# Kernel optimization log

Hardware: AMD Instinct MI355X
Metric: run time of the kernel (lower is better)

Reference implementation:

```python
import jax, jax.numpy as jnp
import numpy as np

N_NODES = 4096
N_EDGES = 500000
N_PAIRS = 2000000
EDGE_DIM = 16
MAX_PATH = 5


def setup_inputs() -> dict:
    key = jax.random.key(0)
    k1, k2, k3, k4, k5 = jax.random.split(key, 5)
    x = jax.random.normal(k1, (N_NODES, EDGE_DIM), dtype=jnp.float32)
    edge_attr = jax.random.normal(k2, (N_EDGES, EDGE_DIM), dtype=jnp.float32)
    path_idx = jax.random.randint(k3, (N_PAIRS, MAX_PATH), 0, N_EDGES, dtype=jnp.int64)
    path_lens = jax.random.randint(k4, (N_PAIRS,), 0, MAX_PATH + 1, dtype=jnp.int64)
    pair_id = jnp.arange(N_PAIRS, dtype=jnp.int64)
    # learned parameter: edge_weights [max_path_distance, edge_dim]
    edge_weights = jax.random.normal(k5, (MAX_PATH, EDGE_DIM), dtype=jnp.float32)
    return {"x": x, "edge_attr": edge_attr, "edge_weights": edge_weights,
            "path_idx": path_idx, "path_lens": path_lens, "pair_id": pair_id}


def reference(x, edge_attr, edge_weights, path_idx, path_lens, pair_id):
    N = x.shape[0]
    L = edge_weights.shape[0]  # max_path_distance
    # valid-position mask for each ragged path, padded to length L
    mask = (jnp.arange(L)[None, :] < path_lens[:, None]).astype(edge_attr.dtype)  # [P, L]
    gathered = edge_attr[path_idx]  # [P, L, D] ragged gather of edge features
    # per-hop dot with learned per-hop weight vector, i.e. (w_l * e_l).sum(dim=1)
    dots = jnp.einsum('pld,ld->pl', gathered, edge_weights)  # [P, L]
    s = jnp.sum(dots * mask, axis=1)  # [P]
    cnt = path_lens.astype(edge_attr.dtype)
    # mean over valid hops; empty path -> NaN in torch -> nan_to_num -> 0
    mean = jnp.where(cnt > 0, s / jnp.maximum(cnt, 1.0), jnp.zeros_like(s))
    src = pair_id % N
    dst = pair_id // N  # unique (src, dst) pairs by construction
    cij = jnp.zeros((N, N), dtype=edge_attr.dtype).at[src, dst].set(mean)
    return cij
```

## Files before the change

kernel.cpp:

```cpp
#include <hip/hip_runtime.h>
#include <hip/hip_fp16.h>

#define NNODES 4096
#define NEDGES 500000
#define NPAIRS 2000000
#define EDIM   16
#define LMAX   5

typedef int v4i __attribute__((ext_vector_type(4)));
typedef float v4f __attribute__((ext_vector_type(4)));

__device__ __forceinline__ v4i ntload4(const int* p) {
  return __builtin_nontemporal_load((const v4i*)p);
}
__device__ __forceinline__ void ntstore4(float* p, float x, float y, float z, float w) {
  v4f t = {x, y, z, w};
  __builtin_nontemporal_store(t, (v4f*)p);
}

#define GLL(gp, lp) __builtin_amdgcn_global_load_lds(                      \
    (const __attribute__((address_space(1))) uint32_t*)(gp),               \
    (__attribute__((address_space(3))) uint32_t*)(lp), 4, 0, 0)

#define DBLOCKS ((NEDGES / 2 + 255) / 256)
#define ZBLOCKS 16384

__global__ __launch_bounds__(256) void prep_kernel(
    const float* __restrict__ edge_attr,
    const float* __restrict__ ew,
    __half* __restrict__ dots,
    float* __restrict__ out) {
  __shared__ float w[LMAX * EDIM];
  const int tid = threadIdx.x, bid = blockIdx.x;

  if (bid >= DBLOCKS) {
    int z = bid - DBLOCKS;
    ntstore4(out + ((size_t)z * 256 + tid) * 4, 0.f, 0.f, 0.f, 0.f);
    return;
  }

  if (tid < LMAX * EDIM) w[tid] = ew[tid];
  __syncthreads();

  int e0 = (bid * 256 + tid) * 2;
  if (e0 >= NEDGES) return;

  const float4* ra = (const float4*)(edge_attr + (size_t)e0 * EDIM);
  float4 a0 = ra[0], a1 = ra[1], a2 = ra[2], a3 = ra[3];
  float4 b0 = ra[4], b1 = ra[5], b2 = ra[6], b3 = ra[7];
  float va[16] = {a0.x, a0.y, a0.z, a0.w, a1.x, a1.y, a1.z, a1.w,
                  a2.x, a2.y, a2.z, a2.w, a3.x, a3.y, a3.z, a3.w};
  float vb[16] = {b0.x, b0.y, b0.z, b0.w, b1.x, b1.y, b1.z, b1.w,
                  b2.x, b2.y, b2.z, b2.w, b3.x, b3.y, b3.z, b3.w};
#pragma unroll
  for (int l = 0; l < LMAX; ++l) {
    float da = 0.f, db = 0.f;
#pragma unroll
    for (int k = 0; k < EDIM; ++k) {
      da += va[k] * w[l * EDIM + k];
      db += vb[k] * w[l * EDIM + k];
    }
    __half2 h;
    h.x = __float2half(da);
    h.y = __float2half(db);
    *(__half2*)(dots + (size_t)l * NEDGES + e0) = h;
  }
}

__device__ __forceinline__ void issue5(const uint32_t* gdots, uint32_t* lbase,
                                       int len, int i0, int i1, int i2, int i3, int i4) {
  uint32_t e0 = (len > 0) ? (uint32_t)i0 : 0u;
  uint32_t e1 = (len > 1) ? (uint32_t)(1 * NEDGES + i1) : 0u;
  uint32_t e2 = (len > 2) ? (uint32_t)(2 * NEDGES + i2) : 0u;
  uint32_t e3 = (len > 3) ? (uint32_t)(3 * NEDGES + i3) : 0u;
  uint32_t e4 = (len > 4) ? (uint32_t)(4 * NEDGES + i4) : 0u;
  GLL(gdots + (e0 >> 1), lbase + 0 * 64);
  GLL(gdots + (e1 >> 1), lbase + 1 * 64);
  GLL(gdots + (e2 >> 1), lbase + 2 * 64);
  GLL(gdots + (e3 >> 1), lbase + 3 * 64);
  GLL(gdots + (e4 >> 1), lbase + 4 * 64);
}

__device__ __forceinline__ float pick(uint32_t dw, int elem) {
  unsigned short u = (unsigned short)((elem & 1) ? (dw >> 16) : (dw & 0xffffu));
  return __half2float(__ushort_as_half(u));
}

__device__ __forceinline__ float sum5(const uint32_t* lbase, int lane, int len,
                                      int i0, int i1, int i2, int i3, int i4) {
  float v0 = pick(lbase[0 * 64 + lane], i0);
  float v1 = pick(lbase[1 * 64 + lane], i1);
  float v2 = pick(lbase[2 * 64 + lane], i2);
  float v3 = pick(lbase[3 * 64 + lane], i3);
  float v4 = pick(lbase[4 * 64 + lane], i4);
  float s = (((len > 0) ? v0 : 0.f) + ((len > 1) ? v1 : 0.f)) +
            (((len > 2) ? v2 : 0.f) + ((len > 3) ? v3 : 0.f)) +
            ((len > 4) ? v4 : 0.f);
  return s / (float)max(len, 1);
}

#define NHEAVY 1024

__global__ __launch_bounds__(256, 3) void fused_mean_transpose(
    const int* __restrict__ path_idx,
    const int* __restrict__ path_lens,
    const __half* __restrict__ dots,
    float* __restrict__ out) {
  __shared__ float tile[64][33];
  __shared__ uint32_t gbuf[4][40][64];
  const int bid = blockIdx.x;
  const int tid = threadIdx.x;
  const int wave = tid >> 6, lane = tid & 63;

  const int tt = bid >> 1;
  const int h  = bid & 1;
  const int dst0 = (tt & 7) * 64 + h * 32;
  const int src0 = (tt >> 3) * 64;
  const uint32_t* gdots = (const uint32_t*)dots;

  {
    const int a = tid >> 4;
    const int c = tid & 15;
    int p0 = (dst0 + a) * NNODES + src0 + 4 * c;
    int p1 = p0 + 16 * NNODES;
    float valid0 = (p0 < NPAIRS) ? 1.f : 0.f;
    float valid1 = (p1 < NPAIRS) ? 1.f : 0.f;
    int pc0 = min(p0, NPAIRS - 4);
    int pc1 = min(p1, NPAIRS - 4);

    const int* q0 = path_idx + (size_t)pc0 * LMAX;
    const int* q1 = path_idx + (size_t)pc1 * LMAX;
    v4i ln0 = ntload4(path_lens + pc0);
    v4i A0 = ntload4(q0);
    v4i B0 = ntload4(q0 + 4);
    v4i C0 = ntload4(q0 + 8);
    v4i D0 = ntload4(q0 + 12);
    v4i E0 = ntload4(q0 + 16);
    v4i ln1 = ntload4(path_lens + pc1);
    v4i A1 = ntload4(q1);
    v4i B1 = ntload4(q1 + 4);
    v4i C1 = ntload4(q1 + 8);
    v4i D1 = ntload4(q1 + 12);
    v4i E1 = ntload4(q1 + 16);
    __builtin_amdgcn_sched_barrier(0);

    int L0 = min(max(ln0[0], 0), LMAX), L1 = min(max(ln0[1], 0), LMAX);
    int L2 = min(max(ln0[2], 0), LMAX), L3 = min(max(ln0[3], 0), LMAX);
    int L4 = min(max(ln1[0], 0), LMAX), L5 = min(max(ln1[1], 0), LMAX);
    int L6 = min(max(ln1[2], 0), LMAX), L7 = min(max(ln1[3], 0), LMAX);

    issue5(gdots, &gbuf[wave][0][0],  L0, A0[0], A0[1], A0[2], A0[3], B0[0]);
    issue5(gdots, &gbuf[wave][5][0],  L1, B0[1], B0[2], B0[3], C0[0], C0[1]);
    issue5(gdots, &gbuf[wave][10][0], L2, C0[2], C0[3], D0[0], D0[1], D0[2]);
    issue5(gdots, &gbuf[wave][15][0], L3, D0[3], E0[0], E0[1], E0[2], E0[3]);
    issue5(gdots, &gbuf[wave][20][0], L4, A1[0], A1[1], A1[2], A1[3], B1[0]);
    issue5(gdots, &gbuf[wave][25][0], L5, B1[1], B1[2], B1[3], C1[0], C1[1]);
    issue5(gdots, &gbuf[wave][30][0], L6, C1[2], C1[3], D1[0], D1[1], D1[2]);
    issue5(gdots, &gbuf[wave][35][0], L7, D1[3], E1[0], E1[1], E1[2], E1[3]);
    asm volatile("s_waitcnt vmcnt(0)" ::: "memory");
    __builtin_amdgcn_sched_barrier(0);

    float4 v0, v1;
    v0.x = sum5(&gbuf[wave][0][0],  lane, L0, A0[0], A0[1], A0[2], A0[3], B0[0]) * valid0;
    v0.y = sum5(&gbuf[wave][5][0],  lane, L1, B0[1], B0[2], B0[3], C0[0], C0[1]) * valid0;
    v0.z = sum5(&gbuf[wave][10][0], lane, L2, C0[2], C0[3], D0[0], D0[1], D0[2]) * valid0;
    v0.w = sum5(&gbuf[wave][15][0], lane, L3, D0[3], E0[0], E0[1], E0[2], E0[3]) * valid0;
    v1.x = sum5(&gbuf[wave][20][0], lane, L4, A1[0], A1[1], A1[2], A1[3], B1[0]) * valid1;
    v1.y = sum5(&gbuf[wave][25][0], lane, L5, B1[1], B1[2], B1[3], C1[0], C1[1]) * valid1;
    v1.z = sum5(&gbuf[wave][30][0], lane, L6, C1[2], C1[3], D1[0], D1[1], D1[2]) * valid1;
    v1.w = sum5(&gbuf[wave][35][0], lane, L7, D1[3], E1[0], E1[1], E1[2], E1[3]) * valid1;

    tile[4 * c + 0][a] = v0.x;
    tile[4 * c + 1][a] = v0.y;
    tile[4 * c + 2][a] = v0.z;
    tile[4 * c + 3][a] = v0.w;
    tile[4 * c + 0][a + 16] = v1.x;
    tile[4 * c + 1][a + 16] = v1.y;
    tile[4 * c + 2][a + 16] = v1.z;
    tile[4 * c + 3][a + 16] = v1.w;
  }
  __syncthreads();
  {
    const int r  = tid >> 2;
    const int cc = tid & 3;
    float x0 = tile[r][4 * cc + 0];
    float y0 = tile[r][4 * cc + 1];
    float z0 = tile[r][4 * cc + 2];
    float w0 = tile[r][4 * cc + 3];
    float x1 = tile[r][16 + 4 * cc + 0];
    float y1 = tile[r][16 + 4 * cc + 1];
    float z1 = tile[r][16 + 4 * cc + 2];
    float w1 = tile[r][16 + 4 * cc + 3];
    float* o = out + (size_t)(src0 + r) * NNODES + dst0;
    ntstore4(o + 4 * cc, x0, y0, z0, w0);
    ntstore4(o + 16 + 4 * cc, x1, y1, z1, w1);
  }
}

__global__ __launch_bounds__(256) void scatter_kernel(
    const float* __restrict__ edge_attr,
    const float* __restrict__ ew,
    const int* __restrict__ path_idx,
    const int* __restrict__ path_lens,
    float* __restrict__ out) {
  __shared__ float w[LMAX * EDIM];
  if (threadIdx.x < LMAX * EDIM) w[threadIdx.x] = ew[threadIdx.x];
  __syncthreads();

  int p = blockIdx.x * 256 + threadIdx.x;
  if (p >= NPAIRS) return;

  int len = path_lens[p];
  len = min(max(len, 0), LMAX);

  const int* row = path_idx + (size_t)p * LMAX;
  float s = 0.f;
  for (int l = 0; l < len; ++l) {
    int idx = row[l];
    const float4* r = (const float4*)(edge_attr + (size_t)idx * EDIM);
    float4 a0 = r[0], a1 = r[1], a2 = r[2], a3 = r[3];
    const float* wl = &w[l * EDIM];
    s += a0.x * wl[0] + a0.y * wl[1] + a0.z * wl[2] + a0.w * wl[3] +
         a1.x * wl[4] + a1.y * wl[5] + a1.z * wl[6] + a1.w * wl[7] +
         a2.x * wl[8] + a2.y * wl[9] + a2.z * wl[10] + a2.w * wl[11] +
         a3.x * wl[12] + a3.y * wl[13] + a3.z * wl[14] + a3.w * wl[15];
  }
  float m = (len > 0) ? (s / (float)len) : 0.f;
  int src = p & (NNODES - 1);
  int dst = p >> 12;
  out[(size_t)src * NNODES + dst] = m;
}

extern "C" void kernel_launch(void* const* d_in, const int* in_sizes, int n_in,
                              void* d_out, int out_size, void* d_ws, size_t ws_size,
                              hipStream_t stream) {
  const float* edge_attr = (const float*)d_in[1];
  const float* edge_w    = (const float*)d_in[2];
  const int*   path_idx  = (const int*)d_in[3];
  const int*   path_lens = (const int*)d_in[4];
  float* out = (float*)d_out;

  const size_t need = (size_t)LMAX * NEDGES * sizeof(__half);

  if (ws_size >= need) {
    __half* dots = (__half*)d_ws;

    prep_kernel<<<DBLOCKS + ZBLOCKS, 256, 0, stream>>>(edge_attr, edge_w, dots, out);
    fused_mean_transpose<<<NHEAVY, 256, 0, stream>>>(path_idx, path_lens, dots, out);
  } else {
    hipMemsetAsync(d_out, 0, (size_t)out_size * sizeof(float), stream);
    scatter_kernel<<<(NPAIRS + 255) / 256, 256, 0, stream>>>(
        edge_attr, edge_w, path_idx, path_lens, out);
  }
}
```

Baseline: 174.8 us.

## Double-buffer per-hop dot gathers into LDS to shrink shared memory footprint

Replaces the one-shot issue of all 40 global-to-LDS gathers per wave with a hop-by-hop loop. Each loop step issues 8 gathers into one of two LDS buffers while the previous hop is consumed, using a partial vmcnt wait. This cuts the per-wave LDS buffer from 40 to 16 rows, and the launch bound is raised to 4 blocks per CU for more occupancy. The cost is serialized latency across the 5 hops and extra waits, which could lower memory-level parallelism per wave.

```diff
diff --git a/kernel.cpp b/kernel.cpp
--- a/kernel.cpp
+++ b/kernel.cpp
@@ -67,47 +67,15 @@
   }
 }
 
-__device__ __forceinline__ void issue5(const uint32_t* gdots, uint32_t* lbase,
-                                       int len, int i0, int i1, int i2, int i3, int i4) {
-  uint32_t e0 = (len > 0) ? (uint32_t)i0 : 0u;
-  uint32_t e1 = (len > 1) ? (uint32_t)(1 * NEDGES + i1) : 0u;
-  uint32_t e2 = (len > 2) ? (uint32_t)(2 * NEDGES + i2) : 0u;
-  uint32_t e3 = (len > 3) ? (uint32_t)(3 * NEDGES + i3) : 0u;
-  uint32_t e4 = (len > 4) ? (uint32_t)(4 * NEDGES + i4) : 0u;
-  GLL(gdots + (e0 >> 1), lbase + 0 * 64);
-  GLL(gdots + (e1 >> 1), lbase + 1 * 64);
-  GLL(gdots + (e2 >> 1), lbase + 2 * 64);
-  GLL(gdots + (e3 >> 1), lbase + 3 * 64);
-  GLL(gdots + (e4 >> 1), lbase + 4 * 64);
-}
-
-__device__ __forceinline__ float pick(uint32_t dw, int elem) {
-  unsigned short u = (unsigned short)((elem & 1) ? (dw >> 16) : (dw & 0xffffu));
-  return __half2float(__ushort_as_half(u));
-}
-
-__device__ __forceinline__ float sum5(const uint32_t* lbase, int lane, int len,
-                                      int i0, int i1, int i2, int i3, int i4) {
-  float v0 = pick(lbase[0 * 64 + lane], i0);
-  float v1 = pick(lbase[1 * 64 + lane], i1);
-  float v2 = pick(lbase[2 * 64 + lane], i2);
-  float v3 = pick(lbase[3 * 64 + lane], i3);
-  float v4 = pick(lbase[4 * 64 + lane], i4);
-  float s = (((len > 0) ? v0 : 0.f) + ((len > 1) ? v1 : 0.f)) +
-            (((len > 2) ? v2 : 0.f) + ((len > 3) ? v3 : 0.f)) +
-            ((len > 4) ? v4 : 0.f);
-  return s / (float)max(len, 1);
-}
-
 #define NHEAVY 1024
 
-__global__ __launch_bounds__(256, 3) void fused_mean_transpose(
+__global__ __launch_bounds__(256, 4) void fused_mean_transpose(
     const int* __restrict__ path_idx,
     const int* __restrict__ path_lens,
     const __half* __restrict__ dots,
     float* __restrict__ out) {
   __shared__ float tile[64][33];
-  __shared__ uint32_t gbuf[4][40][64];
+  __shared__ uint32_t gbuf[4][2][8][64];
   const int bid = blockIdx.x;
   const int tid = threadIdx.x;
   const int wave = tid >> 6, lane = tid & 63;
@@ -142,33 +110,69 @@
     v4i C1 = ntload4(q1 + 8);
     v4i D1 = ntload4(q1 + 12);
     v4i E1 = ntload4(q1 + 16);
-    __builtin_amdgcn_sched_barrier(0);
-
-    int L0 = min(max(ln0[0], 0), LMAX), L1 = min(max(ln0[1], 0), LMAX);
-    int L2 = min(max(ln0[2], 0), LMAX), L3 = min(max(ln0[3], 0), LMAX);
-    int L4 = min(max(ln1[0], 0), LMAX), L5 = min(max(ln1[1], 0), LMAX);
-    int L6 = min(max(ln1[2], 0), LMAX), L7 = min(max(ln1[3], 0), LMAX);
-
-    issue5(gdots, &gbuf[wave][0][0],  L0, A0[0], A0[1], A0[2], A0[3], B0[0]);
-    issue5(gdots, &gbuf[wave][5][0],  L1, B0[1], B0[2], B0[3], C0[0], C0[1]);
-    issue5(gdots, &gbuf[wave][10][0], L2, C0[2], C0[3], D0[0], D0[1], D0[2]);
-    issue5(gdots, &gbuf[wave][15][0], L3, D0[3], E0[0], E0[1], E0[2], E0[3]);
-    issue5(gdots, &gbuf[wave][20][0], L4, A1[0], A1[1], A1[2], A1[3], B1[0]);
-    issue5(gdots, &gbuf[wave][25][0], L5, B1[1], B1[2], B1[3], C1[0], C1[1]);
-    issue5(gdots, &gbuf[wave][30][0], L6, C1[2], C1[3], D1[0], D1[1], D1[2]);
-    issue5(gdots, &gbuf[wave][35][0], L7, D1[3], E1[0], E1[1], E1[2], E1[3]);
+
+    int f[8][LMAX];
+#pragma unroll
+    for (int k = 0; k < 4; ++k) {
+      f[0][k] = A0[k]; f[4][k] = A1[k];
+      f[1][k + 1] = B0[k + 1 > 3 ? 0 : 0], f[1][k] = 0;
+    }
+    f[0][0]=A0[0]; f[0][1]=A0[1]; f[0][2]=A0[2]; f[0][3]=A0[3]; f[0][4]=B0[0];
+    f[1][0]=B0[1]; f[1][1]=B0[2]; f[1][2]=B0[3]; f[1][3]=C0[0]; f[1][4]=C0[1];
+    f[2][0]=C0[2]; f[2][1]=C0[3]; f[2][2]=D0[0]; f[2][3]=D0[1]; f[2][4]=D0[2];
+    f[3][0]=D0[3]; f[3][1]=E0[0]; f[3][2]=E0[1]; f[3][3]=E0[2]; f[3][4]=E0[3];
+    f[4][0]=A1[0]; f[4][1]=A1[1]; f[4][2]=A1[2]; f[4][3]=A1[3]; f[4][4]=B1[0];
+    f[5][0]=B1[1]; f[5][1]=B1[2]; f[5][2]=B1[3]; f[5][3]=C1[0]; f[5][4]=C1[1];
+    f[6][0]=C1[2]; f[6][1]=C1[3]; f[6][2]=D1[0]; f[6][3]=D1[1]; f[6][4]=D1[2];
+    f[7][0]=D1[3]; f[7][1]=E1[0]; f[7][2]=E1[1]; f[7][3]=E1[2]; f[7][4]=E1[3];
+
+    int L[8];
+    L[0]=min(max(ln0[0],0),LMAX); L[1]=min(max(ln0[1],0),LMAX);
+    L[2]=min(max(ln0[2],0),LMAX); L[3]=min(max(ln0[3],0),LMAX);
+    L[4]=min(max(ln1[0],0),LMAX); L[5]=min(max(ln1[1],0),LMAX);
+    L[6]=min(max(ln1[2],0),LMAX); L[7]=min(max(ln1[3],0),LMAX);
+
     asm volatile("s_waitcnt vmcnt(0)" ::: "memory");
-    __builtin_amdgcn_sched_barrier(0);
+
+#pragma unroll
+    for (int j = 0; j < 8; ++j) {
+      uint32_t e = (L[j] > 0) ? (uint32_t)f[j][0] : 0u;
+      GLL(gdots + (e >> 1), &gbuf[wave][0][j][0]);
+    }
+    float s[8] = {0.f, 0.f, 0.f, 0.f, 0.f, 0.f, 0.f, 0.f};
+#pragma unroll
+    for (int l = 0; l < LMAX; ++l) {
+      if (l + 1 < LMAX) {
+#pragma unroll
+        for (int j = 0; j < 8; ++j) {
+          uint32_t e = (L[j] > l + 1)
+              ? (uint32_t)((l + 1) * NEDGES + f[j][l + 1]) : 0u;
+          GLL(gdots + (e >> 1), &gbuf[wave][(l + 1) & 1][j][0]);
+        }
+        asm volatile("s_waitcnt vmcnt(8)" ::: "memory");
+      } else {
+        asm volatile("s_waitcnt vmcnt(0)" ::: "memory");
+      }
+      __builtin_amdgcn_sched_barrier(0);
+#pragma unroll
+      for (int j = 0; j < 8; ++j) {
+        uint32_t dw = gbuf[wave][l & 1][j][lane];
+        unsigned short u = (unsigned short)((f[j][l] & 1) ? (dw >> 16)
+                                                          : (dw & 0xffffu));
+        float v = __half2float(__ushort_as_half(u));
+        s[j] += (L[j] > l) ? v : 0.f;
+      }
+    }
 
     float4 v0, v1;
-    v0.x = sum5(&gbuf[wave][0][0],  lane, L0, A0[0], A0[1], A0[2], A0[3], B0[0]) * valid0;
-    v0.y = sum5(&gbuf[wave][5][0],  lane, L1, B0[1], B0[2], B0[3], C0[0], C0[1]) * valid0;
-    v0.z = sum5(&gbuf[wave][10][0], lane, L2, C0[2], C0[3], D0[0], D0[1], D0[2]) * valid0;
-    v0.w = sum5(&gbuf[wave][15][0], lane, L3, D0[3], E0[0], E0[1], E0[2], E0[3]) * valid0;
-    v1.x = sum5(&gbuf[wave][20][0], lane, L4, A1[0], A1[1], A1[2], A1[3], B1[0]) * valid1;
-    v1.y = sum5(&gbuf[wave][25][0], lane, L5, B1[1], B1[2], B1[3], C1[0], C1[1]) * valid1;
-    v1.z = sum5(&gbuf[wave][30][0], lane, L6, C1[2], C1[3], D1[0], D1[1], D1[2]) * valid1;
-    v1.w = sum5(&gbuf[wave][35][0], lane, L7, D1[3], E1[0], E1[1], E1[2], E1[3]) * valid1;
+    v0.x = s[0] / (float)max(L[0], 1) * valid0;
+    v0.y = s[1] / (float)max(L[1], 1) * valid0;
+    v0.z = s[2] / (float)max(L[2], 1) * valid0;
+    v0.w = s[3] / (float)max(L[3], 1) * valid0;
+    v1.x = s[4] / (float)max(L[4], 1) * valid1;
+    v1.y = s[5] / (float)max(L[5], 1) * valid1;
+    v1.z = s[6] / (float)max(L[6], 1) * valid1;
+    v1.w = s[7] / (float)max(L[7], 1) * valid1;
 
     tile[4 * c + 0][a] = v0.x;
     tile[4 * c + 1][a] = v0.y;
```

Measured after the change: 174.3 us. About the same (-0.3%).
